# Optimization experiments

Hardware: AMD Instinct MI355X
Metric: run time of the kernel (lower is better)

The kernel has to match this reference:

```python
import jax, jax.numpy as jnp
import numpy as np

B, N, M = 262144, 8, 4  # batch, state dim, measurement dim


def _psd(key, b, d, scale):
    # SPD matrix: A @ A^T / d + 0.1*I  (keeps inverse well-conditioned)
    A = jax.random.normal(key, (b, d, d), dtype=jnp.float32) * scale
    return A @ A.swapaxes(-1, -2) / d + 0.1 * jnp.eye(d, dtype=jnp.float32)


def setup_inputs() -> dict:
    key = jax.random.key(0)
    kF, kH, kS, kQ, kR = jax.random.split(key, 5)
    F = jax.random.normal(kF, (B, N, N), dtype=jnp.float32) * 0.3 + jnp.eye(N, dtype=jnp.float32)
    H = jax.random.normal(kH, (B, M, N), dtype=jnp.float32) * 0.5
    Sigma_previous = _psd(kS, B, N, 1.0)
    Q = _psd(kQ, B, N, 0.3)
    R = _psd(kR, B, M, 0.3)
    return {"F": F, "H": H, "Sigma_previous": Sigma_previous, "Q": Q, "R": R}


def reference(F, H, Sigma_previous, Q, R):
    T = lambda x: x.swapaxes(-1, -2)
    # predicted state covariance: Sigma = F Sigma_prev F^T + Q        [B,N,N]
    Sigma = F @ Sigma_previous @ T(F) + Q
    # innovation covariance: S = H Sigma H^T + R                      [B,M,M]
    S = H @ Sigma @ T(H) + R
    # Kalman gain: KG = Sigma H^T S^{-1}                              [B,N,M]
    P12 = Sigma @ T(H)
    KG = P12 @ jnp.linalg.inv(S)
    return KG
```

## Files before the change

### kernel.cpp

```cpp
#include <hip/hip_runtime.h>


#define NBB 64
#define THREADS 256

__device__ __forceinline__ void gl_lds16(const float* src, float4* dst) {
    __builtin_amdgcn_global_load_lds(
        (const __attribute__((address_space(1))) unsigned int*)src,
        (__attribute__((address_space(3))) unsigned int*)dst,
        16, 0, 0);
}

__global__ __launch_bounds__(THREADS) void kalman_gain_kernel(
    const float* __restrict__ Fg, const float* __restrict__ Hg,
    const float* __restrict__ Spg, const float* __restrict__ Qg,
    const float* __restrict__ Rg, float* __restrict__ out, int nb)
{
    __shared__ float4 smem4[2600];

    const int tid  = threadIdx.x;
    const int wid  = tid >> 6;
    const int lane = tid & 63;
    const int b0   = blockIdx.x * NBB;

    #pragma unroll
    for (int r4 = 0; r4 < 4; ++r4) {
        int r = r4 * 4 + wid;
        gl_lds16(Fg + (size_t)(b0 + 4 * r) * 64 + lane * 4, smem4 + r * 65);
    }
    #pragma unroll
    for (int r2 = 0; r2 < 2; ++r2) {
        int r = r2 * 4 + wid;
        gl_lds16(Hg + (size_t)(b0 + 8 * r) * 32 + lane * 4, smem4 + 2080 + r * 65);
    }
    #pragma unroll
    for (int r4 = 0; r4 < 4; ++r4) {
        int r = r4 * 4 + wid;
        gl_lds16(Spg + (size_t)(b0 + 4 * r) * 64 + lane * 4, smem4 + 1040 + r * 65);
    }

    const int b_loc = tid >> 2;
    const int p     = tid & 3;
    const int baseF  = (b_loc >> 2) * 65 + (b_loc & 3) * 16;
    const int baseSp = 1040 + baseF;
    const int baseH  = 2080 + (b_loc >> 3) * 65 + (b_loc & 7) * 8;

    const float4 Rr = *(reinterpret_cast<const float4*>(Rg)
                        + (size_t)(b0 + b_loc) * 4 + p);

    __syncthreads();

    float hs[8];
    #pragma unroll
    for (int j = 0; j < 4; ++j) {
        float4 v = smem4[baseH + 2 * j + (p >> 1)];
        hs[j*2+0] = (p & 1) ? v.z : v.x;
        hs[j*2+1] = (p & 1) ? v.w : v.y;
    }

    float fr[16];
    #pragma unroll
    for (int i = 0; i < 4; ++i) {
        float4 v = smem4[baseF + 4 * p + i];
        fr[i*4+0] = v.x; fr[i*4+1] = v.y; fr[i*4+2] = v.z; fr[i*4+3] = v.w;
    }

    float u[32];
    #pragma unroll
    for (int x = 0; x < 32; ++x) u[x] = 0.f;
    #pragma unroll
    for (int rl = 0; rl < 2; ++rl)
        #pragma unroll
        for (int k = 0; k < 8; ++k)
            #pragma unroll
            for (int j = 0; j < 4; ++j)
                u[k*4+j] += hs[j*2+rl] * fr[rl*8+k];
    #pragma unroll
    for (int x = 0; x < 32; ++x) u[x] += __shfl_xor(u[x], 1, 64);
    #pragma unroll
    for (int x = 0; x < 32; ++x) u[x] += __shfl_xor(u[x], 2, 64);

    __syncthreads();

    #pragma unroll
    for (int r4 = 0; r4 < 4; ++r4) {
        int r = r4 * 4 + wid;
        gl_lds16(Qg + (size_t)(b0 + 4 * r) * 64 + lane * 4, smem4 + r * 65);
    }

    float G[16];
    #pragma unroll
    for (int x = 0; x < 16; ++x) G[x] = 0.f;
    #pragma unroll
    for (int k = 0; k < 8; ++k) {
        float4 s0 = smem4[baseSp + 2*k    ];
        float4 s1 = smem4[baseSp + 2*k + 1];
        float sp[8] = {s0.x,s0.y,s0.z,s0.w, s1.x,s1.y,s1.z,s1.w};
        #pragma unroll
        for (int il = 0; il < 2; ++il)
            #pragma unroll
            for (int c = 0; c < 8; ++c)
                G[il*8+c] += fr[il*8+k] * sp[c];
    }

    float A[8];
    #pragma unroll
    for (int il = 0; il < 2; ++il)
        #pragma unroll
        for (int j = 0; j < 4; ++j) {
            float acc = 0.f;
            #pragma unroll
            for (int k = 0; k < 8; ++k)
                acc += G[il*8+k] * u[k*4+j];
            A[il*4+j] = acc;
        }

    __syncthreads();

    float qo[16];
    #pragma unroll
    for (int i = 0; i < 4; ++i) {
        float4 v = smem4[baseF + 4 * p + i];
        qo[i*4+0] = v.x; qo[i*4+1] = v.y; qo[i*4+2] = v.z; qo[i*4+3] = v.w;
    }
    #pragma unroll
    for (int j = 0; j < 4; ++j) {
        float4 h0 = smem4[baseH + 2*j    ];
        float4 h1 = smem4[baseH + 2*j + 1];
        float hrow[8] = {h0.x,h0.y,h0.z,h0.w, h1.x,h1.y,h1.z,h1.w};
        #pragma unroll
        for (int il = 0; il < 2; ++il) {
            float acc = 0.f;
            #pragma unroll
            for (int k = 0; k < 8; ++k)
                acc += qo[il*8+k] * hrow[k];
            A[il*4+j] += acc;
        }
    }

    float s[16];
    #pragma unroll
    for (int pi = 0; pi < 4; ++pi) {
        float rrow[4] = {Rr.x, Rr.y, Rr.z, Rr.w};
        #pragma unroll
        for (int q = 0; q < 4; ++q) {
            float acc = (pi == p) ? rrow[q] : 0.f;
            #pragma unroll
            for (int il = 0; il < 2; ++il)
                acc += hs[pi*2+il] * A[il*4+q];
            s[pi*4+q] = acc;
        }
    }
    #pragma unroll
    for (int x = 0; x < 16; ++x) s[x] += __shfl_xor(s[x], 1, 64);
    #pragma unroll
    for (int x = 0; x < 16; ++x) s[x] += __shfl_xor(s[x], 2, 64);

    float is[16] = {1.f,0.f,0.f,0.f, 0.f,1.f,0.f,0.f, 0.f,0.f,1.f,0.f, 0.f,0.f,0.f,1.f};
    #pragma unroll
    for (int c = 0; c < 4; ++c) {
        float pinv = 1.0f / s[c*4+c];
        #pragma unroll
        for (int k = 0; k < 4; ++k) { s[c*4+k] *= pinv; is[c*4+k] *= pinv; }
        #pragma unroll
        for (int r = 0; r < 4; ++r) {
            if (r != c) {
                float fac = s[r*4+c];
                #pragma unroll
                for (int k = 0; k < 4; ++k) {
                    s[r*4+k]  -= fac * s[c*4+k];
                    is[r*4+k] -= fac * is[c*4+k];
                }
            }
        }
    }

    float4* outg = reinterpret_cast<float4*>(out)
                 + (size_t)(b0 + b_loc) * 8 + 2 * p;
    #pragma unroll
    for (int il = 0; il < 2; ++il) {
        float4 o;
        o.x = A[il*4+0]*is[0] + A[il*4+1]*is[4] + A[il*4+2]*is[8]  + A[il*4+3]*is[12];
        o.y = A[il*4+0]*is[1] + A[il*4+1]*is[5] + A[il*4+2]*is[9]  + A[il*4+3]*is[13];
        o.z = A[il*4+0]*is[2] + A[il*4+1]*is[6] + A[il*4+2]*is[10] + A[il*4+3]*is[14];
        o.w = A[il*4+0]*is[3] + A[il*4+1]*is[7] + A[il*4+2]*is[11] + A[il*4+3]*is[15];
        outg[il] = o;
    }
}

extern "C" void kernel_launch(void* const* d_in, const int* in_sizes, int n_in,
                              void* d_out, int out_size, void* d_ws, size_t ws_size,
                              hipStream_t stream) {
    const float* F  = (const float*)d_in[0];
    const float* H  = (const float*)d_in[1];
    const float* Sp = (const float*)d_in[2];
    const float* Q  = (const float*)d_in[3];
    const float* R  = (const float*)d_in[4];
    float* out = (float*)d_out;

    int nb = in_sizes[0] / 64;
    int blocks = nb / NBB;
    kalman_gain_kernel<<<blocks, THREADS, 0, stream>>>(F, H, Sp, Q, R, out, nb);
}
```

Before: 51.31 us.

## Shrink blocks to one wave, prefetch all inputs up front, nontemporal stores

Each block now holds a single 64-thread wave covering 16 batches instead of 256 threads covering 64. All inputs (F, Sigma_prev, H, Q, R) are issued as async global-to-LDS loads at the start, so the mid-kernel barriers and the reuse of F's buffer for Q are gone. R now comes through LDS as well. Output stores use nontemporal hints. This removes the barrier stalls and serialized Q loads and gives more independent blocks, at the cost of four times as many blocks and less compute available to hide each block's load latency.

```diff
diff --git a/kernel.cpp b/kernel.cpp
--- a/kernel.cpp
+++ b/kernel.cpp
@@ -1,8 +1,10 @@
 #include <hip/hip_runtime.h>
 
 
-#define NBB 64
-#define THREADS 256
+#define NBB 16
+#define THREADS 64
+
+typedef float floatx4 __attribute__((ext_vector_type(4)));
 
 __device__ __forceinline__ void gl_lds16(const float* src, float4* dst) {
     __builtin_amdgcn_global_load_lds(
@@ -16,39 +18,35 @@
     const float* __restrict__ Spg, const float* __restrict__ Qg,
     const float* __restrict__ Rg, float* __restrict__ out, int nb)
 {
-    __shared__ float4 smem4[2600];
+    __shared__ float4 smem4[974];
 
-    const int tid  = threadIdx.x;
-    const int wid  = tid >> 6;
-    const int lane = tid & 63;
+    const int lane = threadIdx.x;
     const int b0   = blockIdx.x * NBB;
 
     #pragma unroll
-    for (int r4 = 0; r4 < 4; ++r4) {
-        int r = r4 * 4 + wid;
+    for (int r = 0; r < 4; ++r)
         gl_lds16(Fg + (size_t)(b0 + 4 * r) * 64 + lane * 4, smem4 + r * 65);
-    }
     #pragma unroll
-    for (int r2 = 0; r2 < 2; ++r2) {
-        int r = r2 * 4 + wid;
-        gl_lds16(Hg + (size_t)(b0 + 8 * r) * 32 + lane * 4, smem4 + 2080 + r * 65);
-    }
+    for (int r = 0; r < 4; ++r)
+        gl_lds16(Spg + (size_t)(b0 + 4 * r) * 64 + lane * 4, smem4 + 260 + r * 65);
     #pragma unroll
-    for (int r4 = 0; r4 < 4; ++r4) {
-        int r = r4 * 4 + wid;
-        gl_lds16(Spg + (size_t)(b0 + 4 * r) * 64 + lane * 4, smem4 + 1040 + r * 65);
-    }
+    for (int r = 0; r < 2; ++r)
+        gl_lds16(Hg + (size_t)(b0 + 8 * r) * 32 + lane * 4, smem4 + 520 + r * 65);
+    #pragma unroll
+    for (int r = 0; r < 4; ++r)
+        gl_lds16(Qg + (size_t)(b0 + 4 * r) * 64 + lane * 4, smem4 + 650 + r * 65);
+    gl_lds16(Rg + (size_t)b0 * 16 + lane * 4, smem4 + 910);
 
-    const int b_loc = tid >> 2;
-    const int p     = tid & 3;
+    const int b_loc = lane >> 2;
+    const int p     = lane & 3;
     const int baseF  = (b_loc >> 2) * 65 + (b_loc & 3) * 16;
-    const int baseSp = 1040 + baseF;
-    const int baseH  = 2080 + (b_loc >> 3) * 65 + (b_loc & 7) * 8;
-
-    const float4 Rr = *(reinterpret_cast<const float4*>(Rg)
-                        + (size_t)(b0 + b_loc) * 4 + p);
+    const int baseSp = 260 + baseF;
+    const int baseH  = 520 + (b_loc >> 3) * 65 + (b_loc & 7) * 8;
+    const int baseQ  = 650 + baseF;
 
     __syncthreads();
+
+    const float4 Rr = smem4[910 + lane];
 
     float hs[8];
     #pragma unroll
@@ -80,14 +78,6 @@
     #pragma unroll
     for (int x = 0; x < 32; ++x) u[x] += __shfl_xor(u[x], 2, 64);
 
-    __syncthreads();
-
-    #pragma unroll
-    for (int r4 = 0; r4 < 4; ++r4) {
-        int r = r4 * 4 + wid;
-        gl_lds16(Qg + (size_t)(b0 + 4 * r) * 64 + lane * 4, smem4 + r * 65);
-    }
-
     float G[16];
     #pragma unroll
     for (int x = 0; x < 16; ++x) G[x] = 0.f;
@@ -115,12 +105,10 @@
             A[il*4+j] = acc;
         }
 
-    __syncthreads();
-
     float qo[16];
     #pragma unroll
     for (int i = 0; i < 4; ++i) {
-        float4 v = smem4[baseF + 4 * p + i];
+        float4 v = smem4[baseQ + 4 * p + i];
         qo[i*4+0] = v.x; qo[i*4+1] = v.y; qo[i*4+2] = v.z; qo[i*4+3] = v.w;
     }
     #pragma unroll
@@ -175,16 +163,16 @@
         }
     }
 
-    float4* outg = reinterpret_cast<float4*>(out)
-                 + (size_t)(b0 + b_loc) * 8 + 2 * p;
+    floatx4* outg = reinterpret_cast<floatx4*>(out)
+                  + (size_t)(b0 + b_loc) * 8 + 2 * p;
     #pragma unroll
     for (int il = 0; il < 2; ++il) {
-        float4 o;
+        floatx4 o;
         o.x = A[il*4+0]*is[0] + A[il*4+1]*is[4] + A[il*4+2]*is[8]  + A[il*4+3]*is[12];
         o.y = A[il*4+0]*is[1] + A[il*4+1]*is[5] + A[il*4+2]*is[9]  + A[il*4+3]*is[13];
         o.z = A[il*4+0]*is[2] + A[il*4+1]*is[6] + A[il*4+2]*is[10] + A[il*4+3]*is[14];
         o.w = A[il*4+0]*is[3] + A[il*4+1]*is[7] + A[il*4+2]*is[11] + A[il*4+3]*is[15];
-        outg[il] = o;
+        __builtin_nontemporal_store(o, outg + il);
     }
 }
 
```

New measurement: 49.29 us. -3.9%, faster.
